# Performance work log

Hardware: AMD Instinct MI355X
Metric: run time of the kernel (lower is better)

The kernel has to match this reference:

```python
import jax, jax.numpy as jnp
import numpy as np

B, C, H, W = 256, 512, 14, 14  # C = rnn_size
S = 7                          # spp_size

def setup_inputs() -> dict:
    key = jax.random.key(0)
    ks = jax.random.split(key, 8)
    sd = 1.0 / np.sqrt(C)
    return {
        "att_v": jax.random.normal(ks[0], (B, C, H, W), dtype=jnp.float32),
        "h": jax.random.normal(ks[1], (B, C), dtype=jnp.float32),
        # a2a: Linear(rnn_size, rnn_size)
        "Wa": jax.random.uniform(ks[2], (C, C), jnp.float32, -sd, sd),
        "ba": jax.random.uniform(ks[3], (C,), jnp.float32, -sd, sd),
        # h2a: Linear(rnn_size, rnn_size)
        "Wh": jax.random.uniform(ks[4], (C, C), jnp.float32, -sd, sd),
        "bh": jax.random.uniform(ks[5], (C,), jnp.float32, -sd, sd),
        # d2d: Linear(rnn_size, 1)
        "Wd": jax.random.uniform(ks[6], (C,), jnp.float32, -sd, sd),
        "bd": jax.random.uniform(ks[7], (1,), jnp.float32, -sd, sd),
    }

def reference(att_v, h, Wa, ba, Wh, bh, Wd, bd):
    b, c, hh, ww = att_v.shape
    # AdaptiveAvgPool2d(S) with H,W divisible by S -> block mean
    pooled = att_v.reshape(b, c, S, hh // S, S, ww // S).mean(axis=(3, 5))  # [B,C,S,S]
    a = pooled.reshape(b, c, S * S).transpose(0, 2, 1)  # [B, N=49, C]
    av = jnp.einsum('bnc,dc->bnd', a, Wa) + ba          # a2a, torch Linear: x @ W.T + b
    ah = h @ Wh.T + bh                                  # h2a, [B,C]
    dot = jnp.tanh(av + ah[:, None, :])                 # broadcast add + tanh
    scores = jnp.einsum('bnd,d->bn', dot, Wd) + bd[0]   # d2d -> [B, N]
    weight = jax.nn.softmax(scores, axis=-1)            # over attention positions
    att_res = jnp.einsum('bnc,bn->bc', a, weight)       # bmm(att^T, weight)
    return att_res
```

## Files before the change

### kernel.cpp

```cpp
#include <hip/hip_runtime.h>
#include <hip/hip_bf16.h>

#define BATCH 256
#define CDIM  512
#define NPOS  49
#define MROWS 12544
#define ASTRIDE 520

typedef __attribute__((ext_vector_type(8))) short bf16x8_t;
typedef __attribute__((ext_vector_type(4))) float f32x4_t;

#define WS_NEED 14295040u

__device__ __forceinline__ void load_lds16(const void* g, void* l) {
    __builtin_amdgcn_global_load_lds(
        (const __attribute__((address_space(1))) void*)g,
        (__attribute__((address_space(3))) void*)l, 16, 0, 0);
}

__global__ __launch_bounds__(256, 6) void k1_pool_prep_ah(
    const float* __restrict__ att_v,
    const float* __restrict__ h,
    const float* __restrict__ Wa,
    const float* __restrict__ Wh,
    const float* __restrict__ ba, const float* __restrict__ bh,
    __hip_bfloat16* __restrict__ pooled,
    __hip_bfloat16* __restrict__ Wab,
    float* __restrict__ ahb) {
    __shared__ float4 lds4[32 * 49];
    const int bid = blockIdx.x;
    const int t   = threadIdx.x;

    if (bid < 4096) {
        const int b  = bid >> 4;
        const int cg = bid & 15;
        const float4* src = (const float4*)(att_v + ((size_t)b * CDIM + cg * 32) * 196);
        #pragma unroll
        for (int k = 0; k < 7; ++k) {
            int idx = t + k * 256;
            if (idx < 1568) lds4[idx] = src[idx];
        }
        __syncthreads();
        const int i = t >> 5;
        const int c = t & 31;
        if (i < 7) {
            const float4* fp = &lds4[c * 49 + 7 * i];
            float4 f0 = fp[0], f1 = fp[1], f2 = fp[2], f3 = fp[3];
            float4 f4 = fp[4], f5 = fp[5], f6 = fp[6];
            float p[7];
            p[0] = f0.x + f0.y + f3.z + f3.w;
            p[1] = f0.z + f0.w + f4.x + f4.y;
            p[2] = f1.x + f1.y + f4.z + f4.w;
            p[3] = f1.z + f1.w + f5.x + f5.y;
            p[4] = f2.x + f2.y + f5.z + f5.w;
            p[5] = f2.z + f2.w + f6.x + f6.y;
            p[6] = f3.x + f3.y + f6.z + f6.w;
            __hip_bfloat16* outp =
                pooled + ((size_t)b * NPOS + i * 7) * CDIM + cg * 32 + c;
            #pragma unroll
            for (int j = 0; j < 7; ++j)
                outp[(size_t)j * CDIM] = __float2bfloat16(p[j] * 0.25f);
        }
    } else if (bid < 4352) {
        const int idx = (bid - 4096) * 256 + t;
        float4 v = ((const float4*)Wa)[idx];
        Wab[idx * 4 + 0] = __float2bfloat16(v.x);
        Wab[idx * 4 + 1] = __float2bfloat16(v.y);
        Wab[idx * 4 + 2] = __float2bfloat16(v.z);
        Wab[idx * 4 + 3] = __float2bfloat16(v.w);
    } else {
        const int rel = bid - 4352;
        const int mt = rel & 3;
        const int nt = rel >> 2;
        const int m0 = mt * 64, n0 = nt * 64;
        __hip_bfloat16* aT = (__hip_bfloat16*)lds4;
        __hip_bfloat16* bT = (__hip_bfloat16*)lds4 + 2048;
        const int wave = t >> 6, lane = t & 63;
        const int wm = wave & 1, wn = wave >> 1;
        const int q = lane >> 4, r = lane & 15;
        const int row = t >> 2, cseg = (t & 3) * 8;
        const float* hg = h  + (size_t)(m0 + row) * CDIM + cseg;
        const float* wg = Wh + (size_t)(n0 + row) * CDIM + cseg;

        f32x4_t acc[2][2];
        #pragma unroll
        for (int rt = 0; rt < 2; ++rt)
            #pragma unroll
            for (int ct = 0; ct < 2; ++ct) acc[rt][ct] = (f32x4_t){0.f, 0.f, 0.f, 0.f};

        for (int ks = 0; ks < 16; ++ks) {
            float4 a0 = *(const float4*)(hg + ks * 32);
            float4 a1 = *(const float4*)(hg + ks * 32 + 4);
            float4 b0 = *(const float4*)(wg + ks * 32);
            float4 b1 = *(const float4*)(wg + ks * 32 + 4);
            union { bf16x8_t v; __hip_bfloat16 e[8]; } ua, ub;
            ua.e[0] = __float2bfloat16(a0.x); ua.e[1] = __float2bfloat16(a0.y);
            ua.e[2] = __float2bfloat16(a0.z); ua.e[3] = __float2bfloat16(a0.w);
            ua.e[4] = __float2bfloat16(a1.x); ua.e[5] = __float2bfloat16(a1.y);
            ua.e[6] = __float2bfloat16(a1.z); ua.e[7] = __float2bfloat16(a1.w);
            ub.e[0] = __float2bfloat16(b0.x); ub.e[1] = __float2bfloat16(b0.y);
            ub.e[2] = __float2bfloat16(b0.z); ub.e[3] = __float2bfloat16(b0.w);
            ub.e[4] = __float2bfloat16(b1.x); ub.e[5] = __float2bfloat16(b1.y);
            ub.e[6] = __float2bfloat16(b1.z); ub.e[7] = __float2bfloat16(b1.w);
            __syncthreads();
            *(bf16x8_t*)&aT[row * 32 + cseg] = ua.v;
            *(bf16x8_t*)&bT[row * 32 + cseg] = ub.v;
            __syncthreads();
            bf16x8_t af[2], bf[2];
            #pragma unroll
            for (int rt = 0; rt < 2; ++rt)
                af[rt] = *(const bf16x8_t*)&aT[(wm * 32 + rt * 16 + r) * 32 + q * 8];
            #pragma unroll
            for (int ct = 0; ct < 2; ++ct)
                bf[ct] = *(const bf16x8_t*)&bT[(wn * 32 + ct * 16 + r) * 32 + q * 8];
            #pragma unroll
            for (int rt = 0; rt < 2; ++rt)
                #pragma unroll
                for (int ct = 0; ct < 2; ++ct)
                    acc[rt][ct] = __builtin_amdgcn_mfma_f32_16x16x32_bf16(
                        af[rt], bf[ct], acc[rt][ct], 0, 0, 0);
        }
        #pragma unroll
        for (int ct = 0; ct < 2; ++ct) {
            const int col = n0 + wn * 32 + ct * 16 + r;
            const float bias = ba[col] + bh[col];
            #pragma unroll
            for (int rt = 0; rt < 2; ++rt)
                #pragma unroll
                for (int rg = 0; rg < 4; ++rg) {
                    const int orow = m0 + wm * 32 + rt * 16 + q * 4 + rg;
                    ahb[(size_t)orow * CDIM + col] = acc[rt][ct][rg] + bias;
                }
        }
    }
}

__global__ __launch_bounds__(256, 4) void gemm_score(
    const __hip_bfloat16* __restrict__ A,
    const __hip_bfloat16* __restrict__ Bw,
    const float* __restrict__ ahb,
    const float* __restrict__ Wd,
    float* __restrict__ scores8) {
    __shared__ __hip_bfloat16 aT[2 * 64 * 32];
    __shared__ __hip_bfloat16 bT[2 * 128 * 32];
    const int b  = blockIdx.x >> 2;
    const int nt = blockIdx.x & 3;
    const int t = threadIdx.x;
    const int wave = t >> 6, lane = t & 63;
    const int wm = wave & 1, wn = wave >> 1;
    const int q = lane >> 4, r = lane & 15;
    const int m0 = b * NPOS;
    const int n0 = nt * 128;

    const __hip_bfloat16* Ag  = A  + (size_t)(m0 + (t >> 2)) * CDIM + (t & 3) * 8;
    const __hip_bfloat16* Bg0 = Bw + (size_t)(n0 + (t >> 2)) * CDIM + (t & 3) * 8;
    const __hip_bfloat16* Bg1 = Bw + (size_t)(n0 + 64 + (t >> 2)) * CDIM + (t & 3) * 8;
    char* aD = (char*)aT + t * 16;
    char* bD = (char*)bT + t * 16;

    f32x4_t acc[2][4];
    #pragma unroll
    for (int rt = 0; rt < 2; ++rt)
        #pragma unroll
        for (int ct = 0; ct < 4; ++ct) acc[rt][ct] = (f32x4_t){0.f, 0.f, 0.f, 0.f};

    for (int ks = 0; ks < 8; ++ks) {
        const int k0 = ks * 64;
        load_lds16(Ag + k0, aD);
        load_lds16(Ag + k0 + 32, aD + 4096);
        load_lds16(Bg0 + k0, bD);
        load_lds16(Bg1 + k0, bD + 4096);
        load_lds16(Bg0 + k0 + 32, bD + 8192);
        load_lds16(Bg1 + k0 + 32, bD + 12288);
        __syncthreads();
        #pragma unroll
        for (int s = 0; s < 2; ++s) {
            const __hip_bfloat16* aS = aT + s * 2048;
            const __hip_bfloat16* bS = bT + s * 4096;
            bf16x8_t af[2], bf[4];
            #pragma unroll
            for (int rt = 0; rt < 2; ++rt)
                af[rt] = *(const bf16x8_t*)&aS[(wm * 32 + rt * 16 + r) * 32 + q * 8];
            #pragma unroll
            for (int ct = 0; ct < 4; ++ct)
                bf[ct] = *(const bf16x8_t*)&bS[(wn * 64 + ct * 16 + r) * 32 + q * 8];
            #pragma unroll
            for (int rt = 0; rt < 2; ++rt)
                #pragma unroll
                for (int ct = 0; ct < 4; ++ct)
                    acc[rt][ct] = __builtin_amdgcn_mfma_f32_16x16x32_bf16(
                        af[rt], bf[ct], acc[rt][ct], 0, 0, 0);
        }
        __syncthreads();
    }

    float rsum[2][4];
    #pragma unroll
    for (int rt = 0; rt < 2; ++rt)
        #pragma unroll
        for (int rg = 0; rg < 4; ++rg) rsum[rt][rg] = 0.f;

    const float* ahp = ahb + (size_t)b * CDIM;
    #pragma unroll
    for (int ct = 0; ct < 4; ++ct) {
        const int col = n0 + wn * 64 + ct * 16 + r;
        const float ah = ahp[col];
        const float wd = Wd[col];
        #pragma unroll
        for (int rt = 0; rt < 2; ++rt)
            #pragma unroll
            for (int rg = 0; rg < 4; ++rg) {
                float x = acc[rt][ct][rg] + ah;
                float e = __expf(2.f * x);
                rsum[rt][rg] += (1.f - 2.f / (e + 1.f)) * wd;
            }
    }
    #pragma unroll
    for (int m = 1; m < 16; m <<= 1)
        #pragma unroll
        for (int rt = 0; rt < 2; ++rt)
            #pragma unroll
            for (int rg = 0; rg < 4; ++rg)
                rsum[rt][rg] += __shfl_xor(rsum[rt][rg], m, 64);
    if (r == 0) {
        float* seg = scores8 + (size_t)(nt * 2 + wn) * MROWS + m0;
        #pragma unroll
        for (int rt = 0; rt < 2; ++rt)
            #pragma unroll
            for (int rg = 0; rg < 4; ++rg) {
                const int row = wm * 32 + rt * 16 + q * 4 + rg;
                if (row < NPOS) seg[row] = rsum[rt][rg];
            }
    }
}

__global__ __launch_bounds__(256) void softmax_wsum(
    const float* __restrict__ scores8, const __hip_bfloat16* __restrict__ pooled,
    float* __restrict__ out) {
    __shared__ float s_lds[NPOS];
    const int b  = blockIdx.x >> 1;
    const int ch = (blockIdx.x & 1) * 256 + threadIdx.x;
    if (threadIdx.x < NPOS) {
        float s = 0.f;
        #pragma unroll
        for (int seg = 0; seg < 8; ++seg)
            s += scores8[(size_t)seg * MROWS + b * NPOS + threadIdx.x];
        s_lds[threadIdx.x] = s;
    }
    __syncthreads();
    float vmax = -3.0e38f;
    #pragma unroll
    for (int n = 0; n < NPOS; ++n) vmax = fmaxf(vmax, s_lds[n]);
    const __hip_bfloat16* Ap = pooled + (size_t)b * NPOS * CDIM + ch;
    float sum = 0.f, accv = 0.f;
    #pragma unroll
    for (int n = 0; n < NPOS; ++n) {
        float e = __expf(s_lds[n] - vmax);
        sum += e;
        accv += e * __bfloat162float(Ap[(size_t)n * CDIM]);
    }
    out[b * CDIM + ch] = accv / sum;
}

__global__ void prep_convert(const float* __restrict__ Wa,
                             const float* __restrict__ Wh,
                             __hip_bfloat16* __restrict__ Wab,
                             __hip_bfloat16* __restrict__ Whb) {
    int gid = blockIdx.x * blockDim.x + threadIdx.x;
    const int quarter = (CDIM * CDIM) / 4;
    const float4* src; __hip_bfloat16* dst; int idx;
    if (gid < quarter) { src = (const float4*)Wa; dst = Wab; idx = gid; }
    else               { src = (const float4*)Wh; dst = Whb; idx = gid - quarter; }
    float4 v = src[idx];
    dst[idx * 4 + 0] = __float2bfloat16(v.x);
    dst[idx * 4 + 1] = __float2bfloat16(v.y);
    dst[idx * 4 + 2] = __float2bfloat16(v.z);
    dst[idx * 4 + 3] = __float2bfloat16(v.w);
}

__global__ __launch_bounds__(512, 2) void att_spp_main(
    const float* __restrict__ att_v, const float* __restrict__ h,
    const float* __restrict__ ba, const float* __restrict__ bh,
    const float* __restrict__ Wd,
    const __hip_bfloat16* __restrict__ Wab, const __hip_bfloat16* __restrict__ Whb,
    float* __restrict__ out) {
    __shared__ __hip_bfloat16 a_lds[64 * ASTRIDE];
    __shared__ __hip_bfloat16 h_lds[CDIM];
    __shared__ float babh_lds[CDIM];
    __shared__ float wd_lds[CDIM];
    __shared__ float scores_lds[64];
    __shared__ float weights_lds[NPOS];
    const int b = blockIdx.x, t = threadIdx.x;
    h_lds[t]    = __float2bfloat16(h[b * CDIM + t]);
    babh_lds[t] = ba[t] + bh[t];
    wd_lds[t]   = Wd[t];
    if (t < 64) scores_lds[t] = 0.f;
    for (int idx = t; idx < (64 - NPOS) * ASTRIDE; idx += 512)
        a_lds[NPOS * ASTRIDE + idx] = __float2bfloat16(0.f);
    {
        const int jj = t & 7, g = t >> 3;
        const float2* att2 = (const float2*)(att_v + (size_t)b * CDIM * 196);
        if (jj < 7) {
            for (int ci = 0; ci < 8; ++ci) {
                const int c = g + (ci << 6), cbase = c * 98;
                #pragma unroll
                for (int i = 0; i < 7; ++i) {
                    float2 v0 = att2[cbase + i * 14 + jj];
                    float2 v1 = att2[cbase + i * 14 + 7 + jj];
                    a_lds[(i * 7 + jj) * ASTRIDE + c] =
                        __float2bfloat16((v0.x + v0.y + v1.x + v1.y) * 0.25f);
                }
            }
        }
    }
    __syncthreads();
    const int wave = t >> 6, lane = t & 63, q = lane >> 4, r = lane & 15;
    f32x4_t acc[4][4];
    #pragma unroll
    for (int rt = 0; rt < 4; ++rt)
        #pragma unroll
        for (int ct = 0; ct < 4; ++ct) acc[rt][ct] = (f32x4_t){0.f,0.f,0.f,0.f};
    const int dBase = wave * 64 + r;
    for (int ks = 0; ks < 16; ++ks) {
        const int k0 = ks * 32 + q * 8;
        bf16x8_t af[4], bf[4];
        #pragma unroll
        for (int rt = 0; rt < 4; ++rt)
            af[rt] = *(const bf16x8_t*)&a_lds[(rt * 16 + r) * ASTRIDE + k0];
        #pragma unroll
        for (int ct = 0; ct < 4; ++ct)
            bf[ct] = *(const bf16x8_t*)&Wab[(size_t)(dBase + ct * 16) * CDIM + k0];
        #pragma unroll
        for (int rt = 0; rt < 4; ++rt)
            #pragma unroll
            for (int ct = 0; ct < 4; ++ct)
                acc[rt][ct] = __builtin_amdgcn_mfma_f32_16x16x32_bf16(
                    af[rt], bf[ct], acc[rt][ct], 0, 0, 0);
    }
    for (int ks = 0; ks < 16; ++ks) {
        const int k0 = ks * 32 + q * 8;
        bf16x8_t af = *(const bf16x8_t*)&h_lds[k0];
        bf16x8_t bf[4];
        #pragma unroll
        for (int ct = 0; ct < 4; ++ct)
            bf[ct] = *(const bf16x8_t*)&Whb[(size_t)(dBase + ct * 16) * CDIM + k0];
        #pragma unroll
        for (int rt = 0; rt < 4; ++rt)
            #pragma unroll
            for (int ct = 0; ct < 4; ++ct)
                acc[rt][ct] = __builtin_amdgcn_mfma_f32_16x16x32_bf16(
                    af, bf[ct], acc[rt][ct], 0, 0, 0);
    }
    float part[4][4];
    #pragma unroll
    for (int rt = 0; rt < 4; ++rt)
        #pragma unroll
        for (int rg = 0; rg < 4; ++rg) part[rt][rg] = 0.f;
    #pragma unroll
    for (int ct = 0; ct < 4; ++ct) {
        const int d = dBase + ct * 16;
        const float bias = babh_lds[d], wd = wd_lds[d];
        #pragma unroll
        for (int rt = 0; rt < 4; ++rt)
            #pragma unroll
            for (int rg = 0; rg < 4; ++rg) {
                float x = acc[rt][ct][rg] + bias;
                float e = __expf(2.f * x);
                part[rt][rg] += (1.f - 2.f / (e + 1.f)) * wd;
            }
    }
    #pragma unroll
    for (int m = 1; m < 16; m <<= 1)
        #pragma unroll
        for (int rt = 0; rt < 4; ++rt)
            #pragma unroll
            for (int rg = 0; rg < 4; ++rg)
                part[rt][rg] += __shfl_xor(part[rt][rg], m, 64);
    if (r == 0) {
        #pragma unroll
        for (int rt = 0; rt < 4; ++rt)
            #pragma unroll
            for (int rg = 0; rg < 4; ++rg)
                atomicAdd(&scores_lds[rt * 16 + q * 4 + rg], part[rt][rg]);
    }
    __syncthreads();
    if (wave == 0) {
        float v = (lane < NPOS) ? scores_lds[lane] : -3.0e38f;
        float vmax = v;
        #pragma unroll
        for (int m = 1; m < 64; m <<= 1) vmax = fmaxf(vmax, __shfl_xor(vmax, m, 64));
        float e = (lane < NPOS) ? __expf(v - vmax) : 0.f;
        float s = e;
        #pragma unroll
        for (int m = 1; m < 64; m <<= 1) s += __shfl_xor(s, m, 64);
        if (lane < NPOS) weights_lds[lane] = e / s;
    }
    __syncthreads();
    float sum = 0.f;
    #pragma unroll
    for (int n = 0; n < NPOS; ++n)
        sum += __bfloat162float(a_lds[n * ASTRIDE + t]) * weights_lds[n];
    out[b * CDIM + t] = sum;
}

extern "C" void kernel_launch(void* const* d_in, const int* in_sizes, int n_in,
                              void* d_out, int out_size, void* d_ws, size_t ws_size,
                              hipStream_t stream) {
    const float* att_v = (const float*)d_in[0];
    const float* h     = (const float*)d_in[1];
    const float* Wa    = (const float*)d_in[2];
    const float* ba    = (const float*)d_in[3];
    const float* Wh    = (const float*)d_in[4];
    const float* bh    = (const float*)d_in[5];
    const float* Wd    = (const float*)d_in[6];

    if (ws_size >= WS_NEED) {
        char* ws = (char*)d_ws;
        __hip_bfloat16* Wab     = (__hip_bfloat16*)(ws);
        __hip_bfloat16* pooled  = (__hip_bfloat16*)(ws + 524288);
        float*          ahb     = (float*)(ws + 13369344);
        float*          scores8 = (float*)(ws + 13893632);

        k1_pool_prep_ah<<<4384, 256, 0, stream>>>(att_v, h, Wa, Wh, ba, bh,
                                                  pooled, Wab, ahb);
        gemm_score<<<1024, 256, 0, stream>>>(pooled, Wab, ahb, Wd, scores8);
        softmax_wsum<<<512, 256, 0, stream>>>(scores8, pooled, (float*)d_out);
    } else {
        __hip_bfloat16* Wab = (__hip_bfloat16*)d_ws;
        __hip_bfloat16* Whb = Wab + (size_t)CDIM * CDIM;
        prep_convert<<<512, 256, 0, stream>>>(Wa, Wh, Wab, Whb);
        att_spp_main<<<BATCH, 512, 0, stream>>>(att_v, h, ba, bh, Wd, Wab, Whb,
                                                (float*)d_out);
    }
}
```

Measured before the change: 197.0 us.

## Fuse softmax-weighted sum into GEMM kernel via last-block atomic counter

Removes the separate softmax_wsum launch: each gemm block bumps a per-batch atomic counter, and the last of the four N-tile blocks for a batch reduces the partial scores, applies the softmax and computes the weighted sum over pooled rows. Counters are zeroed by an extra block in the first kernel, whose block order is also changed so the small Wa-convert and h2a GEMM blocks are scheduled before the pooling blocks. This saves one launch and its gap at the cost of fences, atomics and a serialized tail in one block per batch.

```diff
diff --git a/kernel.cpp b/kernel.cpp
--- a/kernel.cpp
+++ b/kernel.cpp
@@ -10,7 +10,7 @@
 typedef __attribute__((ext_vector_type(8))) short bf16x8_t;
 typedef __attribute__((ext_vector_type(4))) float f32x4_t;
 
-#define WS_NEED 14295040u
+#define WS_NEED 14296064u
 
 __device__ __forceinline__ void load_lds16(const void* g, void* l) {
     __builtin_amdgcn_global_load_lds(
@@ -26,50 +26,23 @@
     const float* __restrict__ ba, const float* __restrict__ bh,
     __hip_bfloat16* __restrict__ pooled,
     __hip_bfloat16* __restrict__ Wab,
-    float* __restrict__ ahb) {
+    float* __restrict__ ahb,
+    int* __restrict__ counters) {
     __shared__ float4 lds4[32 * 49];
     const int bid = blockIdx.x;
     const int t   = threadIdx.x;
 
-    if (bid < 4096) {
-        const int b  = bid >> 4;
-        const int cg = bid & 15;
-        const float4* src = (const float4*)(att_v + ((size_t)b * CDIM + cg * 32) * 196);
-        #pragma unroll
-        for (int k = 0; k < 7; ++k) {
-            int idx = t + k * 256;
-            if (idx < 1568) lds4[idx] = src[idx];
-        }
-        __syncthreads();
-        const int i = t >> 5;
-        const int c = t & 31;
-        if (i < 7) {
-            const float4* fp = &lds4[c * 49 + 7 * i];
-            float4 f0 = fp[0], f1 = fp[1], f2 = fp[2], f3 = fp[3];
-            float4 f4 = fp[4], f5 = fp[5], f6 = fp[6];
-            float p[7];
-            p[0] = f0.x + f0.y + f3.z + f3.w;
-            p[1] = f0.z + f0.w + f4.x + f4.y;
-            p[2] = f1.x + f1.y + f4.z + f4.w;
-            p[3] = f1.z + f1.w + f5.x + f5.y;
-            p[4] = f2.x + f2.y + f5.z + f5.w;
-            p[5] = f2.z + f2.w + f6.x + f6.y;
-            p[6] = f3.x + f3.y + f6.z + f6.w;
-            __hip_bfloat16* outp =
-                pooled + ((size_t)b * NPOS + i * 7) * CDIM + cg * 32 + c;
-            #pragma unroll
-            for (int j = 0; j < 7; ++j)
-                outp[(size_t)j * CDIM] = __float2bfloat16(p[j] * 0.25f);
-        }
-    } else if (bid < 4352) {
-        const int idx = (bid - 4096) * 256 + t;
+    if (bid == 0) {
+        counters[t] = 0;
+    } else if (bid <= 256) {
+        const int idx = (bid - 1) * 256 + t;
         float4 v = ((const float4*)Wa)[idx];
         Wab[idx * 4 + 0] = __float2bfloat16(v.x);
         Wab[idx * 4 + 1] = __float2bfloat16(v.y);
         Wab[idx * 4 + 2] = __float2bfloat16(v.z);
         Wab[idx * 4 + 3] = __float2bfloat16(v.w);
-    } else {
-        const int rel = bid - 4352;
+    } else if (bid <= 288) {
+        const int rel = bid - 257;
         const int mt = rel & 3;
         const int nt = rel >> 2;
         const int m0 = mt * 64, n0 = nt * 64;
@@ -132,17 +105,52 @@
                     ahb[(size_t)orow * CDIM + col] = acc[rt][ct][rg] + bias;
                 }
         }
-    }
-}
-
-__global__ __launch_bounds__(256, 4) void gemm_score(
+    } else {
+        const int rel = bid - 289;
+        const int b  = rel >> 4;
+        const int cg = rel & 15;
+        const float4* src = (const float4*)(att_v + ((size_t)b * CDIM + cg * 32) * 196);
+        #pragma unroll
+        for (int k = 0; k < 7; ++k) {
+            int idx = t + k * 256;
+            if (idx < 1568) lds4[idx] = src[idx];
+        }
+        __syncthreads();
+        const int i = t >> 5;
+        const int c = t & 31;
+        if (i < 7) {
+            const float4* fp = &lds4[c * 49 + 7 * i];
+            float4 f0 = fp[0], f1 = fp[1], f2 = fp[2], f3 = fp[3];
+            float4 f4 = fp[4], f5 = fp[5], f6 = fp[6];
+            float p[7];
+            p[0] = f0.x + f0.y + f3.z + f3.w;
+            p[1] = f0.z + f0.w + f4.x + f4.y;
+            p[2] = f1.x + f1.y + f4.z + f4.w;
+            p[3] = f1.z + f1.w + f5.x + f5.y;
+            p[4] = f2.x + f2.y + f5.z + f5.w;
+            p[5] = f2.z + f2.w + f6.x + f6.y;
+            p[6] = f3.x + f3.y + f6.z + f6.w;
+            __hip_bfloat16* outp =
+                pooled + ((size_t)b * NPOS + i * 7) * CDIM + cg * 32 + c;
+            #pragma unroll
+            for (int j = 0; j < 7; ++j)
+                outp[(size_t)j * CDIM] = __float2bfloat16(p[j] * 0.25f);
+        }
+    }
+}
+
+__global__ __launch_bounds__(256, 4) void gemm_score_fused(
     const __hip_bfloat16* __restrict__ A,
     const __hip_bfloat16* __restrict__ Bw,
     const float* __restrict__ ahb,
     const float* __restrict__ Wd,
-    float* __restrict__ scores8) {
+    float* __restrict__ scores8,
+    int* __restrict__ counters,
+    float* __restrict__ out) {
     __shared__ __hip_bfloat16 aT[2 * 64 * 32];
     __shared__ __hip_bfloat16 bT[2 * 128 * 32];
+    __shared__ float s_w[NPOS];
+    __shared__ int   last_flag;
     const int b  = blockIdx.x >> 2;
     const int nt = blockIdx.x & 3;
     const int t = threadIdx.x;
@@ -232,34 +240,47 @@
                 if (row < NPOS) seg[row] = rsum[rt][rg];
             }
     }
-}
-
-__global__ __launch_bounds__(256) void softmax_wsum(
-    const float* __restrict__ scores8, const __hip_bfloat16* __restrict__ pooled,
-    float* __restrict__ out) {
-    __shared__ float s_lds[NPOS];
-    const int b  = blockIdx.x >> 1;
-    const int ch = (blockIdx.x & 1) * 256 + threadIdx.x;
-    if (threadIdx.x < NPOS) {
+
+    __threadfence();
+    __syncthreads();
+    if (t == 0) last_flag = (atomicAdd(&counters[b], 1) == 3);
+    __syncthreads();
+    if (!last_flag) return;
+    __threadfence();
+
+    if (t < NPOS) {
         float s = 0.f;
         #pragma unroll
         for (int seg = 0; seg < 8; ++seg)
-            s += scores8[(size_t)seg * MROWS + b * NPOS + threadIdx.x];
-        s_lds[threadIdx.x] = s;
-    }
-    __syncthreads();
-    float vmax = -3.0e38f;
-    #pragma unroll
-    for (int n = 0; n < NPOS; ++n) vmax = fmaxf(vmax, s_lds[n]);
-    const __hip_bfloat16* Ap = pooled + (size_t)b * NPOS * CDIM + ch;
-    float sum = 0.f, accv = 0.f;
+            s += scores8[(size_t)seg * MROWS + m0 + t];
+        s_w[t] = s;
+    }
+    __syncthreads();
+    if (t < NPOS) {
+        float vmax = -3.0e38f;
+        #pragma unroll
+        for (int n = 0; n < NPOS; ++n) vmax = fmaxf(vmax, s_w[n]);
+        float S = 0.f;
+        #pragma unroll
+        for (int n = 0; n < NPOS; ++n) S += __expf(s_w[n] - vmax);
+        float e = __expf(s_w[t] - vmax);
+        __syncthreads();
+        s_w[t] = e / S;
+    } else {
+        __syncthreads();
+    }
+    __syncthreads();
+
+    const __hip_bfloat16* Ap = A + (size_t)m0 * CDIM;
+    float a0 = 0.f, a1 = 0.f;
     #pragma unroll
     for (int n = 0; n < NPOS; ++n) {
-        float e = __expf(s_lds[n] - vmax);
-        sum += e;
-        accv += e * __bfloat162float(Ap[(size_t)n * CDIM]);
-    }
-    out[b * CDIM + ch] = accv / sum;
+        const float w = s_w[n];
+        a0 += w * __bfloat162float(Ap[(size_t)n * CDIM + t]);
+        a1 += w * __bfloat162float(Ap[(size_t)n * CDIM + t + 256]);
+    }
+    out[b * CDIM + t]       = a0;
+    out[b * CDIM + t + 256] = a1;
 }
 
 __global__ void prep_convert(const float* __restrict__ Wa,
@@ -420,11 +441,13 @@
         __hip_bfloat16* pooled  = (__hip_bfloat16*)(ws + 524288);
         float*          ahb     = (float*)(ws + 13369344);
         float*          scores8 = (float*)(ws + 13893632);
-
-        k1_pool_prep_ah<<<4384, 256, 0, stream>>>(att_v, h, Wa, Wh, ba, bh,
-                                                  pooled, Wab, ahb);
-        gemm_score<<<1024, 256, 0, stream>>>(pooled, Wab, ahb, Wd, scores8);
-        softmax_wsum<<<512, 256, 0, stream>>>(scores8, pooled, (float*)d_out);
+        int*            counters= (int*)(ws + 14295040);
+
+        k1_pool_prep_ah<<<4385, 256, 0, stream>>>(att_v, h, Wa, Wh, ba, bh,
+                                                  pooled, Wab, ahb, counters);
+        gemm_score_fused<<<1024, 256, 0, stream>>>(pooled, Wab, ahb, Wd,
+                                                   scores8, counters,
+                                                   (float*)d_out);
     } else {
         __hip_bfloat16* Wab = (__hip_bfloat16*)d_ws;
         __hip_bfloat16* Whb = Wab + (size_t)CDIM * CDIM;
```

After: 323.1 us. 64.0% more time.
